# Kernel optimization log

Hardware: AMD Instinct MI355X
Metric: run time of the kernel (lower is better)

The kernel has to match this reference:

```python
import jax, jax.numpy as jnp
import numpy as np

N_NODES = 50000
N_EDGES = 800000
IN_DIM, HID_DIM, OUT_DIM = 128, 256, 64


def setup_inputs() -> dict:
    key = jax.random.key(0)
    k1, k2, k3, k4 = jax.random.split(key, 4)
    x = jax.random.normal(k1, (N_NODES, IN_DIM), dtype=jnp.float32)
    edge_index = jax.random.randint(k2, (2, N_EDGES), 0, N_NODES, dtype=jnp.int32)
    # Glorot-ish scaled weights
    W1 = jax.random.normal(k3, (IN_DIM, HID_DIM), dtype=jnp.float32) * (1.0 / np.sqrt(IN_DIM))
    W2 = jax.random.normal(k4, (HID_DIM, OUT_DIM), dtype=jnp.float32) * (1.0 / np.sqrt(HID_DIM))
    b1 = jnp.zeros((HID_DIM,), dtype=jnp.float32)
    b2 = jnp.zeros((OUT_DIM,), dtype=jnp.float32)
    return {"x": x, "edge_index": edge_index, "W1": W1, "b1": b1, "W2": W2, "b2": b2}


def _gcn_conv(x, src, dst, deg_inv_sqrt, W, b):
    # transform first (PyG GCNConv order), then edge-normalized scatter-add
    h = x @ W                                        # [N, D_out]
    norm = deg_inv_sqrt[src] * deg_inv_sqrt[dst]     # [E]
    msgs = h[src] * norm[:, None]                    # [E, D_out]
    agg = jax.ops.segment_sum(msgs, dst, num_segments=x.shape[0])
    return agg + b


def reference(x, edge_index, W1, b1, W2, b2):
    n = x.shape[0]
    loops = jnp.arange(n, dtype=edge_index.dtype)
    src = jnp.concatenate([edge_index[0], loops])    # add self-loops
    dst = jnp.concatenate([edge_index[1], loops])
    deg = jax.ops.segment_sum(jnp.ones_like(dst, dtype=x.dtype), dst, num_segments=n)
    deg_inv_sqrt = jnp.where(deg > 0, jax.lax.rsqrt(jnp.maximum(deg, 1e-12)), 0.0)
    h = jax.nn.relu(_gcn_conv(x, src, dst, deg_inv_sqrt, W1, b1))
    h = _gcn_conv(h, src, dst, deg_inv_sqrt, W2, b2)
    return jax.nn.log_softmax(h, axis=1)
```

## Files before the change

### kernel.cpp

```cpp
#include <hip/hip_runtime.h>
#include <hip/hip_bf16.h>
#include <math.h>

#define N_NODES 50000
#define N_EDGES 800000
#define IN_DIM 128
#define HID_DIM 256
#define OUT_DIM 64
#define NPART 196
#define CAP 8192
#define CHUNK 2048
#define NPB ((N_EDGES + CHUNK - 1) / CHUNK)

typedef __attribute__((ext_vector_type(8))) short bf16x8;
typedef __attribute__((ext_vector_type(4))) short short4v;
typedef __attribute__((ext_vector_type(4))) float f32x4;

__device__ inline short f2bf(float f) {
    unsigned u = __float_as_uint(f);
    unsigned r = (u + 0x7fffu + ((u >> 16) & 1u)) >> 16;
    return (short)r;
}
__device__ inline float bf_lo(unsigned u) { return __uint_as_float(u << 16); }
__device__ inline float bf_hi(unsigned u) { return __uint_as_float(u & 0xffff0000u); }

__global__ __launch_bounds__(256) void part1_pack_kernel(const int* __restrict__ src,
                                                         const int* __restrict__ dst,
                                                         int* __restrict__ coarseCursor,
                                                         uint2* __restrict__ sedge,
                                                         const float* __restrict__ W1,
                                                         const float* __restrict__ W2,
                                                         short* __restrict__ Bp1,
                                                         short* __restrict__ Bp2, int E) {
    __shared__ int cnt_l[NPART];
    __shared__ int pref[NPART];
    __shared__ int gbase[NPART];
    __shared__ int ws4[4];
    __shared__ uint2 stage[CHUNK];
    int tid = threadIdx.x;
    if (blockIdx.x >= NPB) {
        int idx = (blockIdx.x - NPB) * 256 + tid;
        const float* W; short* Bp; int N;
        const int T1 = (IN_DIM / 32) * (HID_DIM / 16) * 64;
        const int T2 = (HID_DIM / 32) * (OUT_DIM / 16) * 64;
        if (idx < T1) { W = W1; Bp = Bp1; N = HID_DIM; }
        else { idx -= T1; if (idx >= T2) return; W = W2; Bp = Bp2; N = OUT_DIM; }
        int lane = idx & 63;
        int frag = idx >> 6;
        int ntiles = N >> 4;
        int nt = frag % ntiles;
        int kt = frag / ntiles;
        int col = nt * 16 + (lane & 15);
        int krow = kt * 32 + (lane >> 4) * 8;
        bf16x8 pk;
        #pragma unroll
        for (int j = 0; j < 8; j++) pk[j] = f2bf(W[(size_t)(krow + j) * N + col]);
        *((bf16x8*)(Bp + (size_t)idx * 8)) = pk;
        return;
    }
    int e0 = blockIdx.x * CHUNK;
    if (tid < NPART) cnt_l[tid] = 0;
    __syncthreads();
    int es[CHUNK / 256], ed[CHUNK / 256];
    #pragma unroll
    for (int j = 0; j < CHUNK / 256; j++) {
        int e = e0 + j * 256 + tid;
        if (e < E) {
            es[j] = src[e]; ed[j] = dst[e];
            atomicAdd(&cnt_l[ed[j] >> 8], 1);
        } else ed[j] = -1;
    }
    __syncthreads();
    int lane = tid & 63, wid = tid >> 6;
    int v = (tid < NPART) ? cnt_l[tid] : 0;
    int s = v;
    #pragma unroll
    for (int off = 1; off < 64; off <<= 1) {
        int t = __shfl_up(s, off, 64);
        if (lane >= off) s += t;
    }
    if (lane == 63) ws4[wid] = s;
    __syncthreads();
    int wp = 0;
    #pragma unroll
    for (int w = 0; w < 4; w++) wp += (w < wid) ? ws4[w] : 0;
    int excl = s - v + wp;
    if (tid < NPART) pref[tid] = excl;
    __syncthreads();
    if (tid < NPART) cnt_l[tid] = excl;
    __syncthreads();
    #pragma unroll
    for (int j = 0; j < CHUNK / 256; j++) {
        if (ed[j] >= 0) {
            int c = ed[j] >> 8;
            int p = atomicAdd(&cnt_l[c], 1);
            stage[p] = make_uint2((unsigned)es[j], (unsigned)ed[j]);
        }
    }
    __syncthreads();
    if (tid < NPART) {
        int cl = cnt_l[tid] - pref[tid];
        gbase[tid] = (cl > 0) ? (tid * CAP + atomicAdd(&coarseCursor[tid], cl)) : 0;
    }
    __syncthreads();
    int total = (e0 + CHUNK <= E) ? CHUNK : (E - e0);
    for (int i = tid; i < total; i += 256) {
        uint2 ev = stage[i];
        int c = (int)(ev.y >> 8);
        sedge[gbase[c] + (i - pref[c])] = ev;
    }
}

__global__ __launch_bounds__(256) void part2_kernel(const uint2* __restrict__ sedge,
                                                    const int* __restrict__ coarseCnt,
                                                    int* __restrict__ offs,
                                                    int* __restrict__ cntg,
                                                    float* __restrict__ dis,
                                                    int* __restrict__ ssrc,
                                                    const float* __restrict__ x,
                                                    short* __restrict__ xb, int n) {
    __shared__ int kcnt[256];
    __shared__ int ws4[4];
    __shared__ float sdis[256];
    int b = blockIdx.x, tid = threadIdx.x;
    int base = b * CAP;
    int cb = coarseCnt[b];
    kcnt[tid] = 0;
    __syncthreads();
    for (int i = tid; i < cb; i += 256) {
        uint2 ev = sedge[base + i];
        atomicAdd(&kcnt[ev.y & 255], 1);
    }
    __syncthreads();
    int v = kcnt[tid];
    int lane = tid & 63, wid = tid >> 6;
    int s = v;
    #pragma unroll
    for (int off = 1; off < 64; off <<= 1) {
        int t = __shfl_up(s, off, 64);
        if (lane >= off) s += t;
    }
    if (lane == 63) ws4[wid] = s;
    __syncthreads();
    int wp = 0;
    #pragma unroll
    for (int w = 0; w < 4; w++) wp += (w < wid) ? ws4[w] : 0;
    int excl = s - v + wp;
    int node = b * 256 + tid;
    float dn = rsqrtf((float)v + 1.0f);
    if (node < n) {
        offs[node] = base + excl;
        cntg[node] = v;
        dis[node] = dn;
    }
    sdis[tid] = dn;
    __syncthreads();
    kcnt[tid] = base + excl;
    __syncthreads();
    for (int i = tid; i < cb; i += 256) {
        uint2 ev = sedge[base + i];
        int pos = atomicAdd(&kcnt[ev.y & 255], 1);
        ssrc[pos] = (int)ev.x;
    }
    int rlane = tid & 31, rgrp = tid >> 5;
    for (int rb = 0; rb < 32; rb++) {
        int row = rb * 8 + rgrp;
        int nd = b * 256 + row;
        if (nd >= n) break;
        float d2 = sdis[row];
        float4 vv = ((const float4*)(x + (size_t)nd * IN_DIM))[rlane];
        short4v o = {f2bf(vv.x * d2), f2bf(vv.y * d2), f2bf(vv.z * d2), f2bf(vv.w * d2)};
        *((short4v*)(xb + (size_t)nd * IN_DIM + rlane * 4)) = o;
    }
}

__global__ void agg1_kernel(const short* __restrict__ xb, const int* __restrict__ ssrc,
                            const int* __restrict__ offs, const int* __restrict__ cnt,
                            const float* __restrict__ dis, short* __restrict__ aggx, int n) {
    int lane = threadIdx.x & 63;
    int node = blockIdx.x * 4 + (threadIdx.x >> 6);
    if (node >= n) return;
    int grp = lane >> 3, l8 = lane & 7;
    int start = offs[node], c = cnt[node];
    int vidx = (lane < c) ? ssrc[start + lane] : 0;
    float acc[16] = {};
    int lim = (c < 64) ? c : 64;
    int rounds = (lim + 15) >> 4;
    for (int r = 0; r < rounds; r++) {
        int j0 = r * 16 + grp;
        int j1 = j0 + 8;
        int i0 = (j0 < 63) ? j0 : 63;
        int i1 = (j1 < 63) ? j1 : 63;
        int s0 = __shfl(vidx, i0, 64);
        int s1 = __shfl(vidx, i1, 64);
        float g0 = (j0 < lim) ? 1.0f : 0.0f;
        float g1 = (j1 < lim) ? 1.0f : 0.0f;
        const uint4* r0 = (const uint4*)(xb + (size_t)s0 * IN_DIM + l8 * 16);
        const uint4* r1 = (const uint4*)(xb + (size_t)s1 * IN_DIM + l8 * 16);
        uint4 a0 = r0[0], a1 = r0[1];
        uint4 b0 = r1[0], b1 = r1[1];
        acc[0]  += g0 * bf_lo(a0.x); acc[1]  += g0 * bf_hi(a0.x);
        acc[2]  += g0 * bf_lo(a0.y); acc[3]  += g0 * bf_hi(a0.y);
        acc[4]  += g0 * bf_lo(a0.z); acc[5]  += g0 * bf_hi(a0.z);
        acc[6]  += g0 * bf_lo(a0.w); acc[7]  += g0 * bf_hi(a0.w);
        acc[8]  += g0 * bf_lo(a1.x); acc[9]  += g0 * bf_hi(a1.x);
        acc[10] += g0 * bf_lo(a1.y); acc[11] += g0 * bf_hi(a1.y);
        acc[12] += g0 * bf_lo(a1.z); acc[13] += g0 * bf_hi(a1.z);
        acc[14] += g0 * bf_lo(a1.w); acc[15] += g0 * bf_hi(a1.w);
        acc[0]  += g1 * bf_lo(b0.x); acc[1]  += g1 * bf_hi(b0.x);
        acc[2]  += g1 * bf_lo(b0.y); acc[3]  += g1 * bf_hi(b0.y);
        acc[4]  += g1 * bf_lo(b0.z); acc[5]  += g1 * bf_hi(b0.z);
        acc[6]  += g1 * bf_lo(b0.w); acc[7]  += g1 * bf_hi(b0.w);
        acc[8]  += g1 * bf_lo(b1.x); acc[9]  += g1 * bf_hi(b1.x);
        acc[10] += g1 * bf_lo(b1.y); acc[11] += g1 * bf_hi(b1.y);
        acc[12] += g1 * bf_lo(b1.z); acc[13] += g1 * bf_hi(b1.z);
        acc[14] += g1 * bf_lo(b1.w); acc[15] += g1 * bf_hi(b1.w);
    }
    for (int j = 64 + grp; j < c; j += 8) {
        int s0 = ssrc[start + j];
        const uint4* r0 = (const uint4*)(xb + (size_t)s0 * IN_DIM + l8 * 16);
        uint4 a0 = r0[0], a1 = r0[1];
        acc[0]  += bf_lo(a0.x); acc[1]  += bf_hi(a0.x); acc[2]  += bf_lo(a0.y); acc[3]  += bf_hi(a0.y);
        acc[4]  += bf_lo(a0.z); acc[5]  += bf_hi(a0.z); acc[6]  += bf_lo(a0.w); acc[7]  += bf_hi(a0.w);
        acc[8]  += bf_lo(a1.x); acc[9]  += bf_hi(a1.x); acc[10] += bf_lo(a1.y); acc[11] += bf_hi(a1.y);
        acc[12] += bf_lo(a1.z); acc[13] += bf_hi(a1.z); acc[14] += bf_lo(a1.w); acc[15] += bf_hi(a1.w);
    }
    #pragma unroll
    for (int k = 0; k < 16; k++) {
        acc[k] += __shfl_xor(acc[k], 8, 64);
        acc[k] += __shfl_xor(acc[k], 16, 64);
        acc[k] += __shfl_xor(acc[k], 32, 64);
    }
    if (grp == 0) {
        float dn = dis[node];
        const uint4* rs = (const uint4*)(xb + (size_t)node * IN_DIM + l8 * 16);
        uint4 a0 = rs[0], a1 = rs[1];
        acc[0]  += bf_lo(a0.x); acc[1]  += bf_hi(a0.x); acc[2]  += bf_lo(a0.y); acc[3]  += bf_hi(a0.y);
        acc[4]  += bf_lo(a0.z); acc[5]  += bf_hi(a0.z); acc[6]  += bf_lo(a0.w); acc[7]  += bf_hi(a0.w);
        acc[8]  += bf_lo(a1.x); acc[9]  += bf_hi(a1.x); acc[10] += bf_lo(a1.y); acc[11] += bf_hi(a1.y);
        acc[12] += bf_lo(a1.z); acc[13] += bf_hi(a1.z); acc[14] += bf_lo(a1.w); acc[15] += bf_hi(a1.w);
        bf16x8 o0, o1;
        #pragma unroll
        for (int k = 0; k < 8; k++) { o0[k] = f2bf(acc[k] * dn); o1[k] = f2bf(acc[k + 8] * dn); }
        short* dst0 = aggx + (size_t)node * IN_DIM + l8 * 16;
        *((bf16x8*)dst0) = o0;
        *((bf16x8*)(dst0 + 8)) = o1;
    }
}

#define H1_STRIDE 264
__global__ __launch_bounds__(256) void gemm_fused_kernel(const short* __restrict__ A,
                                                         const short* __restrict__ Bp1,
                                                         const short* __restrict__ Bp2,
                                                         const float* __restrict__ b1,
                                                         const float* __restrict__ dis,
                                                         short* __restrict__ h2, int M) {
    __shared__ short lds_h1[4][16][H1_STRIDE];
    int lane = threadIdx.x & 63;
    int w = threadIdx.x >> 6;
    int rowBase = blockIdx.x * 64 + w * 16;
    int arow = rowBase + (lane & 15);
    int kseg = lane >> 4;
    int col0 = lane & 15;

    constexpr int NT1 = HID_DIM / 16;
    f32x4 acc1[NT1] = {};
    #pragma unroll
    for (int kt = 0; kt < IN_DIM / 32; kt++) {
        bf16x8 a = {};
        if (arow < M)
            a = *((const bf16x8*)(A + (size_t)arow * IN_DIM + kt * 32 + kseg * 8));
        #pragma unroll
        for (int nt = 0; nt < NT1; nt++) {
            bf16x8 b = *((const bf16x8*)(Bp1 + ((size_t)(kt * NT1 + nt) * 64 + lane) * 8));
            acc1[nt] = __builtin_amdgcn_mfma_f32_16x16x32_bf16(a, b, acc1[nt], 0, 0, 0);
        }
    }
    #pragma unroll
    for (int nt = 0; nt < NT1; nt++) {
        float bv = b1[nt * 16 + col0];
        #pragma unroll
        for (int i = 0; i < 4; i++) {
            float v = fmaxf(acc1[nt][i] + bv, 0.0f);
            lds_h1[w][kseg * 4 + i][nt * 16 + col0] = f2bf(v);
        }
    }
    constexpr int NT2 = OUT_DIM / 16;
    f32x4 acc2[NT2] = {};
    #pragma unroll
    for (int kt = 0; kt < HID_DIM / 32; kt++) {
        bf16x8 a = *((const bf16x8*)&lds_h1[w][lane & 15][kt * 32 + kseg * 8]);
        #pragma unroll
        for (int nt = 0; nt < NT2; nt++) {
            bf16x8 b = *((const bf16x8*)(Bp2 + ((size_t)(kt * NT2 + nt) * 64 + lane) * 8));
            acc2[nt] = __builtin_amdgcn_mfma_f32_16x16x32_bf16(a, b, acc2[nt], 0, 0, 0);
        }
    }
    #pragma unroll
    for (int i = 0; i < 4; i++) {
        int r = rowBase + kseg * 4 + i;
        if (r >= M) continue;
        float sc = dis[r];
        #pragma unroll
        for (int nt = 0; nt < NT2; nt++)
            h2[(size_t)r * OUT_DIM + nt * 16 + col0] = f2bf(acc2[nt][i] * sc);
    }
}

__global__ void agg2_kernel(const short* __restrict__ h2, const int* __restrict__ ssrc,
                            const int* __restrict__ offs, const int* __restrict__ cnt,
                            const float* __restrict__ dis, const float* __restrict__ b2,
                            float* __restrict__ out, int n) {
    int lane = threadIdx.x & 63;
    int node = blockIdx.x * 4 + (threadIdx.x >> 6);
    if (node >= n) return;
    int grp = lane >> 3, l8 = lane & 7;
    int start = offs[node], c = cnt[node];
    int vidx = (lane < c) ? ssrc[start + lane] : 0;
    float acc[8] = {};
    int lim = (c < 64) ? c : 64;
    int rounds = (lim + 15) >> 4;
    for (int r = 0; r < rounds; r++) {
        int j0 = r * 16 + grp;
        int j1 = j0 + 8;
        int i0 = (j0 < 63) ? j0 : 63;
        int i1 = (j1 < 63) ? j1 : 63;
        int s0 = __shfl(vidx, i0, 64);
        int s1 = __shfl(vidx, i1, 64);
        float g0 = (j0 < lim) ? 1.0f : 0.0f;
        float g1 = (j1 < lim) ? 1.0f : 0.0f;
        uint4 p0 = *((const uint4*)(h2 + (size_t)s0 * OUT_DIM + l8 * 8));
        uint4 p1 = *((const uint4*)(h2 + (size_t)s1 * OUT_DIM + l8 * 8));
        acc[0] += g0 * bf_lo(p0.x); acc[1] += g0 * bf_hi(p0.x);
        acc[2] += g0 * bf_lo(p0.y); acc[3] += g0 * bf_hi(p0.y);
        acc[4] += g0 * bf_lo(p0.z); acc[5] += g0 * bf_hi(p0.z);
        acc[6] += g0 * bf_lo(p0.w); acc[7] += g0 * bf_hi(p0.w);
        acc[0] += g1 * bf_lo(p1.x); acc[1] += g1 * bf_hi(p1.x);
        acc[2] += g1 * bf_lo(p1.y); acc[3] += g1 * bf_hi(p1.y);
        acc[4] += g1 * bf_lo(p1.z); acc[5] += g1 * bf_hi(p1.z);
        acc[6] += g1 * bf_lo(p1.w); acc[7] += g1 * bf_hi(p1.w);
    }
    for (int j = 64 + grp; j < c; j += 8) {
        int s0 = ssrc[start + j];
        uint4 p0 = *((const uint4*)(h2 + (size_t)s0 * OUT_DIM + l8 * 8));
        acc[0] += bf_lo(p0.x); acc[1] += bf_hi(p0.x); acc[2] += bf_lo(p0.y); acc[3] += bf_hi(p0.y);
        acc[4] += bf_lo(p0.z); acc[5] += bf_hi(p0.z); acc[6] += bf_lo(p0.w); acc[7] += bf_hi(p0.w);
    }
    #pragma unroll
    for (int k = 0; k < 8; k++) {
        acc[k] += __shfl_xor(acc[k], 8, 64);
        acc[k] += __shfl_xor(acc[k], 16, 64);
        acc[k] += __shfl_xor(acc[k], 32, 64);
    }
    float dn = dis[node];
    uint4 pv = *((const uint4*)(h2 + (size_t)node * OUT_DIM + l8 * 8));
    float4 bb0 = ((const float4*)b2)[l8 * 2];
    float4 bb1 = ((const float4*)b2)[l8 * 2 + 1];
    acc[0] = (acc[0] + bf_lo(pv.x)) * dn + bb0.x;
    acc[1] = (acc[1] + bf_hi(pv.x)) * dn + bb0.y;
    acc[2] = (acc[2] + bf_lo(pv.y)) * dn + bb0.z;
    acc[3] = (acc[3] + bf_hi(pv.y)) * dn + bb0.w;
    acc[4] = (acc[4] + bf_lo(pv.z)) * dn + bb1.x;
    acc[5] = (acc[5] + bf_hi(pv.z)) * dn + bb1.y;
    acc[6] = (acc[6] + bf_lo(pv.w)) * dn + bb1.z;
    acc[7] = (acc[7] + bf_hi(pv.w)) * dn + bb1.w;
    float m = acc[0];
    #pragma unroll
    for (int k = 1; k < 8; k++) m = fmaxf(m, acc[k]);
    #pragma unroll
    for (int off = 1; off < 8; off <<= 1) m = fmaxf(m, __shfl_xor(m, off, 64));
    float ex = 0.0f;
    #pragma unroll
    for (int k = 0; k < 8; k++) ex += expf(acc[k] - m);
    #pragma unroll
    for (int off = 1; off < 8; off <<= 1) ex += __shfl_xor(ex, off, 64);
    float ls = m + logf(ex);
    if (grp == 0) {
        float4 o0 = {acc[0] - ls, acc[1] - ls, acc[2] - ls, acc[3] - ls};
        float4 o1 = {acc[4] - ls, acc[5] - ls, acc[6] - ls, acc[7] - ls};
        ((float4*)(out + (size_t)node * OUT_DIM))[l8 * 2] = o0;
        ((float4*)(out + (size_t)node * OUT_DIM))[l8 * 2 + 1] = o1;
    }
}

extern "C" void kernel_launch(void* const* d_in, const int* in_sizes, int n_in,
                              void* d_out, int out_size, void* d_ws, size_t ws_size,
                              hipStream_t stream) {
    const float* x  = (const float*)d_in[0];
    const int*   ei = (const int*)d_in[1];
    const float* W1 = (const float*)d_in[2];
    const float* b1 = (const float*)d_in[3];
    const float* W2 = (const float*)d_in[4];
    const float* b2 = (const float*)d_in[5];
    float* out = (float*)d_out;
    char* ws = (char*)d_ws;

    const int* srcp = ei;
    const int* dstp = ei + N_EDGES;

    int*   coarseCursor = (int*)(ws);
    int*   offs   = (int*)(ws + 4096);
    int*   cntg   = (int*)(ws + 262144);
    float* dis    = (float*)(ws + 524288);
    short* Bp1    = (short*)(ws + 786432);
    short* Bp2    = (short*)(ws + 851968);
    int*   ssrc   = (int*)(ws + 917504);
    uint2* sedge  = (uint2*)(ws + 7340032);
    short* aggx   = (short*)(ws + 7340032);
    short* xb     = (short*)(ws + 20185088);
    short* h2     = (short*)(ws + 32985088);

    hipMemsetAsync(coarseCursor, 0, NPART * 4, stream);

    part1_pack_kernel<<<NPB + 24, 256, 0, stream>>>(srcp, dstp, coarseCursor, sedge,
                                                    W1, W2, Bp1, Bp2, N_EDGES);
    part2_kernel<<<NPART, 256, 0, stream>>>(sedge, coarseCursor, offs, cntg, dis, ssrc,
                                            x, xb, N_NODES);
    agg1_kernel<<<(N_NODES + 3) / 4, 256, 0, stream>>>(xb, ssrc, offs, cntg, dis, aggx, N_NODES);
    gemm_fused_kernel<<<(N_NODES + 63) / 64, 256, 0, stream>>>(aggx, Bp1, Bp2, b1, dis,
                                                               h2, N_NODES);
    agg2_kernel<<<(N_NODES + 3) / 4, 256, 0, stream>>>(h2, ssrc, offs, cntg, dis, b2, out, N_NODES);
}
```

Before: 203.0 us.

## Fuse layer-1 neighbor aggregation into the fused GEMM kernel via LDS staging

Removes the separate agg1 kernel. Each wave of the GEMM kernel now aggregates its own 16 nodes one after another and writes the bf16 rows into LDS, which then feed the MFMA GEMM directly. The goal is to drop the global write and read of the intermediate aggx buffer and one kernel launch. The cost is far fewer waves in flight for the latency-bound gather (782 blocks instead of 12500), serial per-node loops inside each wave, and the GEMM's register pressure now applying to the gather phase too.

```diff
diff --git a/kernel.cpp b/kernel.cpp
--- a/kernel.cpp
+++ b/kernel.cpp
@@ -174,102 +174,118 @@
     }
 }
 
-__global__ void agg1_kernel(const short* __restrict__ xb, const int* __restrict__ ssrc,
-                            const int* __restrict__ offs, const int* __restrict__ cnt,
-                            const float* __restrict__ dis, short* __restrict__ aggx, int n) {
-    int lane = threadIdx.x & 63;
-    int node = blockIdx.x * 4 + (threadIdx.x >> 6);
-    if (node >= n) return;
-    int grp = lane >> 3, l8 = lane & 7;
-    int start = offs[node], c = cnt[node];
-    int vidx = (lane < c) ? ssrc[start + lane] : 0;
-    float acc[16] = {};
-    int lim = (c < 64) ? c : 64;
-    int rounds = (lim + 15) >> 4;
-    for (int r = 0; r < rounds; r++) {
-        int j0 = r * 16 + grp;
-        int j1 = j0 + 8;
-        int i0 = (j0 < 63) ? j0 : 63;
-        int i1 = (j1 < 63) ? j1 : 63;
-        int s0 = __shfl(vidx, i0, 64);
-        int s1 = __shfl(vidx, i1, 64);
-        float g0 = (j0 < lim) ? 1.0f : 0.0f;
-        float g1 = (j1 < lim) ? 1.0f : 0.0f;
-        const uint4* r0 = (const uint4*)(xb + (size_t)s0 * IN_DIM + l8 * 16);
-        const uint4* r1 = (const uint4*)(xb + (size_t)s1 * IN_DIM + l8 * 16);
-        uint4 a0 = r0[0], a1 = r0[1];
-        uint4 b0 = r1[0], b1 = r1[1];
-        acc[0]  += g0 * bf_lo(a0.x); acc[1]  += g0 * bf_hi(a0.x);
-        acc[2]  += g0 * bf_lo(a0.y); acc[3]  += g0 * bf_hi(a0.y);
-        acc[4]  += g0 * bf_lo(a0.z); acc[5]  += g0 * bf_hi(a0.z);
-        acc[6]  += g0 * bf_lo(a0.w); acc[7]  += g0 * bf_hi(a0.w);
-        acc[8]  += g0 * bf_lo(a1.x); acc[9]  += g0 * bf_hi(a1.x);
-        acc[10] += g0 * bf_lo(a1.y); acc[11] += g0 * bf_hi(a1.y);
-        acc[12] += g0 * bf_lo(a1.z); acc[13] += g0 * bf_hi(a1.z);
-        acc[14] += g0 * bf_lo(a1.w); acc[15] += g0 * bf_hi(a1.w);
-        acc[0]  += g1 * bf_lo(b0.x); acc[1]  += g1 * bf_hi(b0.x);
-        acc[2]  += g1 * bf_lo(b0.y); acc[3]  += g1 * bf_hi(b0.y);
-        acc[4]  += g1 * bf_lo(b0.z); acc[5]  += g1 * bf_hi(b0.z);
-        acc[6]  += g1 * bf_lo(b0.w); acc[7]  += g1 * bf_hi(b0.w);
-        acc[8]  += g1 * bf_lo(b1.x); acc[9]  += g1 * bf_hi(b1.x);
-        acc[10] += g1 * bf_lo(b1.y); acc[11] += g1 * bf_hi(b1.y);
-        acc[12] += g1 * bf_lo(b1.z); acc[13] += g1 * bf_hi(b1.z);
-        acc[14] += g1 * bf_lo(b1.w); acc[15] += g1 * bf_hi(b1.w);
-    }
-    for (int j = 64 + grp; j < c; j += 8) {
-        int s0 = ssrc[start + j];
-        const uint4* r0 = (const uint4*)(xb + (size_t)s0 * IN_DIM + l8 * 16);
-        uint4 a0 = r0[0], a1 = r0[1];
-        acc[0]  += bf_lo(a0.x); acc[1]  += bf_hi(a0.x); acc[2]  += bf_lo(a0.y); acc[3]  += bf_hi(a0.y);
-        acc[4]  += bf_lo(a0.z); acc[5]  += bf_hi(a0.z); acc[6]  += bf_lo(a0.w); acc[7]  += bf_hi(a0.w);
-        acc[8]  += bf_lo(a1.x); acc[9]  += bf_hi(a1.x); acc[10] += bf_lo(a1.y); acc[11] += bf_hi(a1.y);
-        acc[12] += bf_lo(a1.z); acc[13] += bf_hi(a1.z); acc[14] += bf_lo(a1.w); acc[15] += bf_hi(a1.w);
-    }
-    #pragma unroll
-    for (int k = 0; k < 16; k++) {
-        acc[k] += __shfl_xor(acc[k], 8, 64);
-        acc[k] += __shfl_xor(acc[k], 16, 64);
-        acc[k] += __shfl_xor(acc[k], 32, 64);
-    }
-    if (grp == 0) {
-        float dn = dis[node];
-        const uint4* rs = (const uint4*)(xb + (size_t)node * IN_DIM + l8 * 16);
-        uint4 a0 = rs[0], a1 = rs[1];
-        acc[0]  += bf_lo(a0.x); acc[1]  += bf_hi(a0.x); acc[2]  += bf_lo(a0.y); acc[3]  += bf_hi(a0.y);
-        acc[4]  += bf_lo(a0.z); acc[5]  += bf_hi(a0.z); acc[6]  += bf_lo(a0.w); acc[7]  += bf_hi(a0.w);
-        acc[8]  += bf_lo(a1.x); acc[9]  += bf_hi(a1.x); acc[10] += bf_lo(a1.y); acc[11] += bf_hi(a1.y);
-        acc[12] += bf_lo(a1.z); acc[13] += bf_hi(a1.z); acc[14] += bf_lo(a1.w); acc[15] += bf_hi(a1.w);
-        bf16x8 o0, o1;
-        #pragma unroll
-        for (int k = 0; k < 8; k++) { o0[k] = f2bf(acc[k] * dn); o1[k] = f2bf(acc[k + 8] * dn); }
-        short* dst0 = aggx + (size_t)node * IN_DIM + l8 * 16;
-        *((bf16x8*)dst0) = o0;
-        *((bf16x8*)(dst0 + 8)) = o1;
-    }
-}
-
-#define H1_STRIDE 264
-__global__ __launch_bounds__(256) void gemm_fused_kernel(const short* __restrict__ A,
-                                                         const short* __restrict__ Bp1,
-                                                         const short* __restrict__ Bp2,
-                                                         const float* __restrict__ b1,
-                                                         const float* __restrict__ dis,
-                                                         short* __restrict__ h2, int M) {
-    __shared__ short lds_h1[4][16][H1_STRIDE];
+#define A_STRIDE 136
+#define H_STRIDE 264
+__global__ __launch_bounds__(256) void agg_gemm_kernel(const short* __restrict__ xb,
+                                                       const int* __restrict__ ssrc,
+                                                       const int* __restrict__ offs,
+                                                       const int* __restrict__ cnt,
+                                                       const float* __restrict__ dis,
+                                                       const short* __restrict__ Bp1,
+                                                       const short* __restrict__ Bp2,
+                                                       const float* __restrict__ b1,
+                                                       short* __restrict__ h2, int M) {
+    __shared__ short lds[4][16 * H_STRIDE];
     int lane = threadIdx.x & 63;
     int w = threadIdx.x >> 6;
     int rowBase = blockIdx.x * 64 + w * 16;
-    int arow = rowBase + (lane & 15);
+    int grp = lane >> 3, l8 = lane & 7;
+
+    for (int m = 0; m < 16; m++) {
+        int node = rowBase + m;
+        if (node < M) {
+            int start = offs[node], c = cnt[node];
+            int vidx = (lane < c) ? ssrc[start + lane] : 0;
+            float acc[16] = {};
+            int lim = (c < 64) ? c : 64;
+            int rounds = (lim + 15) >> 4;
+            for (int r = 0; r < rounds; r++) {
+                int j0 = r * 16 + grp;
+                int j1 = j0 + 8;
+                int i0 = (j0 < 63) ? j0 : 63;
+                int i1 = (j1 < 63) ? j1 : 63;
+                int s0 = __shfl(vidx, i0, 64);
+                int s1 = __shfl(vidx, i1, 64);
+                float g0 = (j0 < lim) ? 1.0f : 0.0f;
+                float g1 = (j1 < lim) ? 1.0f : 0.0f;
+                const uint4* r0 = (const uint4*)(xb + (size_t)s0 * IN_DIM + l8 * 16);
+                const uint4* r1 = (const uint4*)(xb + (size_t)s1 * IN_DIM + l8 * 16);
+                uint4 a0 = r0[0], a1 = r0[1];
+                uint4 b0 = r1[0], b1v = r1[1];
+                acc[0]  += g0 * bf_lo(a0.x); acc[1]  += g0 * bf_hi(a0.x);
+                acc[2]  += g0 * bf_lo(a0.y); acc[3]  += g0 * bf_hi(a0.y);
+                acc[4]  += g0 * bf_lo(a0.z); acc[5]  += g0 * bf_hi(a0.z);
+                acc[6]  += g0 * bf_lo(a0.w); acc[7]  += g0 * bf_hi(a0.w);
+                acc[8]  += g0 * bf_lo(a1.x); acc[9]  += g0 * bf_hi(a1.x);
+                acc[10] += g0 * bf_lo(a1.y); acc[11] += g0 * bf_hi(a1.y);
+                acc[12] += g0 * bf_lo(a1.z); acc[13] += g0 * bf_hi(a1.z);
+                acc[14] += g0 * bf_lo(a1.w); acc[15] += g0 * bf_hi(a1.w);
+                acc[0]  += g1 * bf_lo(b0.x); acc[1]  += g1 * bf_hi(b0.x);
+                acc[2]  += g1 * bf_lo(b0.y); acc[3]  += g1 * bf_hi(b0.y);
+                acc[4]  += g1 * bf_lo(b0.z); acc[5]  += g1 * bf_hi(b0.z);
+                acc[6]  += g1 * bf_lo(b0.w); acc[7]  += g1 * bf_hi(b0.w);
+                acc[8]  += g1 * bf_lo(b1v.x); acc[9]  += g1 * bf_hi(b1v.x);
+                acc[10] += g1 * bf_lo(b1v.y); acc[11] += g1 * bf_hi(b1v.y);
+                acc[12] += g1 * bf_lo(b1v.z); acc[13] += g1 * bf_hi(b1v.z);
+                acc[14] += g1 * bf_lo(b1v.w); acc[15] += g1 * bf_hi(b1v.w);
+            }
+            for (int j = 64 + grp; j < c; j += 8) {
+                int s0 = ssrc[start + j];
+                const uint4* r0 = (const uint4*)(xb + (size_t)s0 * IN_DIM + l8 * 16);
+                uint4 a0 = r0[0], a1 = r0[1];
+                acc[0]  += bf_lo(a0.x); acc[1]  += bf_hi(a0.x);
+                acc[2]  += bf_lo(a0.y); acc[3]  += bf_hi(a0.y);
+                acc[4]  += bf_lo(a0.z); acc[5]  += bf_hi(a0.z);
+                acc[6]  += bf_lo(a0.w); acc[7]  += bf_hi(a0.w);
+                acc[8]  += bf_lo(a1.x); acc[9]  += bf_hi(a1.x);
+                acc[10] += bf_lo(a1.y); acc[11] += bf_hi(a1.y);
+                acc[12] += bf_lo(a1.z); acc[13] += bf_hi(a1.z);
+                acc[14] += bf_lo(a1.w); acc[15] += bf_hi(a1.w);
+            }
+            #pragma unroll
+            for (int k = 0; k < 16; k++) {
+                acc[k] += __shfl_xor(acc[k], 8, 64);
+                acc[k] += __shfl_xor(acc[k], 16, 64);
+                acc[k] += __shfl_xor(acc[k], 32, 64);
+            }
+            if (grp == 0) {
+                float dn = dis[node];
+                const uint4* rs = (const uint4*)(xb + (size_t)node * IN_DIM + l8 * 16);
+                uint4 a0 = rs[0], a1 = rs[1];
+                acc[0]  += bf_lo(a0.x); acc[1]  += bf_hi(a0.x);
+                acc[2]  += bf_lo(a0.y); acc[3]  += bf_hi(a0.y);
+                acc[4]  += bf_lo(a0.z); acc[5]  += bf_hi(a0.z);
+                acc[6]  += bf_lo(a0.w); acc[7]  += bf_hi(a0.w);
+                acc[8]  += bf_lo(a1.x); acc[9]  += bf_hi(a1.x);
+                acc[10] += bf_lo(a1.y); acc[11] += bf_hi(a1.y);
+                acc[12] += bf_lo(a1.z); acc[13] += bf_hi(a1.z);
+                acc[14] += bf_lo(a1.w); acc[15] += bf_hi(a1.w);
+                bf16x8 o0, o1;
+                #pragma unroll
+                for (int k = 0; k < 8; k++) {
+                    o0[k] = f2bf(acc[k] * dn);
+                    o1[k] = f2bf(acc[k + 8] * dn);
+                }
+                short* d0 = &lds[w][m * A_STRIDE + l8 * 16];
+                *((bf16x8*)d0) = o0;
+                *((bf16x8*)(d0 + 8)) = o1;
+            }
+        } else if (grp == 0) {
+            bf16x8 z = {};
+            short* d0 = &lds[w][m * A_STRIDE + l8 * 16];
+            *((bf16x8*)d0) = z;
+            *((bf16x8*)(d0 + 8)) = z;
+        }
+    }
+
+    int arowL = lane & 15;
     int kseg = lane >> 4;
     int col0 = lane & 15;
-
     constexpr int NT1 = HID_DIM / 16;
     f32x4 acc1[NT1] = {};
     #pragma unroll
     for (int kt = 0; kt < IN_DIM / 32; kt++) {
-        bf16x8 a = {};
-        if (arow < M)
-            a = *((const bf16x8*)(A + (size_t)arow * IN_DIM + kt * 32 + kseg * 8));
+        bf16x8 a = *((const bf16x8*)&lds[w][arowL * A_STRIDE + kt * 32 + kseg * 8]);
         #pragma unroll
         for (int nt = 0; nt < NT1; nt++) {
             bf16x8 b = *((const bf16x8*)(Bp1 + ((size_t)(kt * NT1 + nt) * 64 + lane) * 8));
@@ -282,14 +298,14 @@
         #pragma unroll
         for (int i = 0; i < 4; i++) {
             float v = fmaxf(acc1[nt][i] + bv, 0.0f);
-            lds_h1[w][kseg * 4 + i][nt * 16 + col0] = f2bf(v);
+            lds[w][(kseg * 4 + i) * H_STRIDE + nt * 16 + col0] = f2bf(v);
         }
     }
     constexpr int NT2 = OUT_DIM / 16;
     f32x4 acc2[NT2] = {};
     #pragma unroll
     for (int kt = 0; kt < HID_DIM / 32; kt++) {
-        bf16x8 a = *((const bf16x8*)&lds_h1[w][lane & 15][kt * 32 + kseg * 8]);
+        bf16x8 a = *((const bf16x8*)&lds[w][arowL * H_STRIDE + kt * 32 + kseg * 8]);
         #pragma unroll
         for (int nt = 0; nt < NT2; nt++) {
             bf16x8 b = *((const bf16x8*)(Bp2 + ((size_t)(kt * NT2 + nt) * 64 + lane) * 8));
@@ -406,7 +422,6 @@
     short* Bp2    = (short*)(ws + 851968);
     int*   ssrc   = (int*)(ws + 917504);
     uint2* sedge  = (uint2*)(ws + 7340032);
-    short* aggx   = (short*)(ws + 7340032);
     short* xb     = (short*)(ws + 20185088);
     short* h2     = (short*)(ws + 32985088);
 
@@ -416,8 +431,7 @@
                                                     W1, W2, Bp1, Bp2, N_EDGES);
     part2_kernel<<<NPART, 256, 0, stream>>>(sedge, coarseCursor, offs, cntg, dis, ssrc,
                                             x, xb, N_NODES);
-    agg1_kernel<<<(N_NODES + 3) / 4, 256, 0, stream>>>(xb, ssrc, offs, cntg, dis, aggx, N_NODES);
-    gemm_fused_kernel<<<(N_NODES + 63) / 64, 256, 0, stream>>>(aggx, Bp1, Bp2, b1, dis,
-                                                               h2, N_NODES);
+    agg_gemm_kernel<<<(N_NODES + 63) / 64, 256, 0, stream>>>(xb, ssrc, offs, cntg, dis,
+                                                             Bp1, Bp2, b1, h2, N_NODES);
     agg2_kernel<<<(N_NODES + 3) / 4, 256, 0, stream>>>(h2, ssrc, offs, cntg, dis, b2, out, N_NODES);
 }
```

Result: slower. 262.0 us (+29.0%).
